# Performance work log

Measured on AMD Instinct MI355X. Metric: run time of the kernel, lower is better.

Reference implementation:

```python
import jax, jax.numpy as jnp
import numpy as np
import math

B, S, E, R = 128, 16, 512, 500  # batch, seq_len, emb_size, relation_num


def setup_inputs() -> dict:
    key = jax.random.key(0)
    ks = jax.random.split(key, 12)
    s = 1.0 / math.sqrt(E)
    emb = jax.random.normal(ks[0], (R + 1, E), jnp.float32) * s
    emb = emb.at[R].set(0.0)  # padding_idx row is zero in torch
    w_ih = jax.random.normal(ks[1], (4 * E, E), jnp.float32) * s
    w_hh = jax.random.normal(ks[2], (4 * E, E), jnp.float32) * s
    b_ih = jax.random.normal(ks[3], (4 * E,), jnp.float32) * s
    b_hh = jax.random.normal(ks[4], (4 * E,), jnp.float32) * s
    fc_w = jax.random.normal(ks[5], (1, E), jnp.float32) * s
    fc_b = jax.random.normal(ks[6], (1,), jnp.float32) * s
    fcq_w = jax.random.normal(ks[7], (E, E), jnp.float32) * s
    fcq_b = jax.random.normal(ks[8], (E,), jnp.float32) * s
    fck_w = jax.random.normal(ks[9], (E, E), jnp.float32) * s
    fck_b = jax.random.normal(ks[10], (E,), jnp.float32) * s
    tokens = jax.random.randint(ks[11], (B, S), 0, R)  # avoid padding idx R
    return dict(tokens=tokens, emb=emb, w_ih=w_ih, w_hh=w_hh, b_ih=b_ih,
                b_hh=b_hh, fc_w=fc_w, fc_b=fc_b, fcq_w=fcq_w, fcq_b=fcq_b,
                fck_w=fck_w, fck_b=fck_b)


def _lstm_pair(x, w_ih, w_hh, b):
    # x: [..., 2, E]; 2-step LSTM from zero state, return final hidden [..., E]
    def cell(xt, h, c):
        g = xt @ w_ih.T + h @ w_hh.T + b
        i, f, gg, o = jnp.split(g, 4, axis=-1)  # torch gate order i,f,g,o
        c = jax.nn.sigmoid(f) * c + jax.nn.sigmoid(i) * jnp.tanh(gg)
        return jax.nn.sigmoid(o) * jnp.tanh(c), c
    z = jnp.zeros_like(x[..., 0, :])
    h1, c1 = cell(x[..., 0, :], z, z)
    h2, _ = cell(x[..., 1, :], h1, c1)
    return h2


def _attention(x, rel_emb, fcq_w, fcq_b, fck_w, fck_b):
    # x: [B,q,E]; keys = [relation embeddings ; x] -> scores [B,q,R+q]
    b = x.shape[0]
    rel = jnp.broadcast_to(rel_emb[None], (b,) + rel_emb.shape)
    kin = jnp.concatenate([rel, x], axis=1)
    k = kin @ fck_w.T + fck_b
    q = x @ fcq_w.T + fcq_b
    return jnp.einsum('bqe,bke->bqk', q, k) / math.sqrt(E)


def _entropy(scores):
    lp = jax.nn.log_softmax(scores, axis=-1)
    return -jnp.sum(jnp.exp(lp) * lp, axis=-1)


def reference(tokens, emb, w_ih, w_hh, b_ih, b_hh, fc_w, fc_b,
              fcq_w, fcq_b, fck_w, fck_b):
    b_lstm = b_ih + b_hh
    rel_emb = emb[:R]  # relation embeddings used as attention keys/values
    cur = emb[tokens]  # [B,S,E]
    bidx = jnp.arange(B)
    losses = []
    for L in range(S, 1, -1):  # lengths processed: S, S-1, ..., 2
        if L > 2:
            # all adjacent pairs, batched 2-step LSTM: [B, L-1, E]
            pairs = jnp.stack([cur[:, :-1], cur[:, 1:]], axis=2)
            h = _lstm_pair(pairs, w_ih, w_hh, b_lstm)
            sc = jax.nn.sigmoid(h @ fc_w.T + fc_b)[..., 0]  # [B, L-1]
            sel = jnp.argmax(sc, axis=-1)  # [B]
            selected = jnp.take_along_axis(h, sel[:, None, None], axis=1)  # [B,1,E]
            scores = _attention(selected, rel_emb, fcq_w, fcq_b, fck_w, fck_b)
            losses.append(_entropy(scores))  # [B,1]
            # weightedAverage: mask is all-False for seq_len==1, plain softmax
            prob = jax.nn.softmax(scores, axis=-1)  # [B,1,R+1]
            all_emb = jnp.concatenate(
                [jnp.broadcast_to(rel_emb[None], (B, R, E)), selected], axis=1)
            merged = jnp.einsum('bqk,bke->bqe', prob, all_emb)[:, 0]  # [B,E]
            # output = inputs.detach().clone(); write merged at sel; drop row sel+1
            base = jax.lax.stop_gradient(cur)
            base = base.at[bidx, sel].set(merged)
            j = jnp.arange(L - 1)[None, :]
            src = j + (j > sel[:, None]).astype(j.dtype)
            cur = jnp.take_along_axis(base, src[:, :, None], axis=1)  # [B,L-1,E]
        else:  # L == 2: plain LSTM over the two tokens
            h = _lstm_pair(cur, w_ih, w_hh, b_lstm)  # [B,E]
            cur = h[:, None, :]
            losses.append(jnp.zeros((B, 1), cur.dtype))
    scores_f = _attention(cur, rel_emb, fcq_w, fcq_b, fck_w, fck_b)  # [B,1,R+1]
    losses.append(_entropy(scores_f))
    loss_tensor = jnp.concatenate(losses, axis=-1)  # [B,S]
    return scores_f[:, 0], loss_tensor
```

## Files before the change

kernel.cpp:

```cpp
#include <hip/hip_runtime.h>
#include <hip/hip_bf16.h>

#define BB 128
#define SS 16
#define EE 512
#define RR 500
#define G4 2048
#define OUT0 64128
#define NSC 501
#define NPAIR 2047
#define NSU 1012

__device__ __forceinline__ float sigm(float x) { return 1.f / (1.f + expf(-x)); }

__device__ float g_blstm[G4];
__device__ float g_blstmr[G4];
__device__ float g_wihr[G4 * EE];
__device__ float g_whhr[G4 * EE];
__device__ float g_fcw[EE + 4];
__device__ float g_qbias[1024];
__device__ float g_Krel[RR * EE];
__device__ float g_cur[BB * SS * EE];
__device__ float g_G[BB * SS * G4];
__device__ float g_h1[BB * SS * EE];
__device__ float g_c1[BB * SS * EE];
__device__ float g_h2[BB * SS * EE];
__device__ float g_sc[BB * SS];
__device__ float g_ent[BB * SS];
__device__ int   g_sel[BB];
__device__ int   g_ord[BB * SS];
__device__ float g_fckwT[EE * EE];
__device__ float g_W2[RR * EE];
__device__ float g_Mx[EE * EE];
__device__ float g_c2[RR + 4];
__device__ float g_v1[EE];
__device__ float g_c0[1];
__device__ float g_su[BB * NSU];

__global__ void k_prep(const float* __restrict__ bih, const float* __restrict__ bhh,
                       const float* __restrict__ fcwv, const float* __restrict__ fcbv,
                       const float* __restrict__ fcqb, const float* __restrict__ fckb) {
    int i = blockIdx.x * blockDim.x + threadIdx.x;
    if (i < G4) g_blstm[i] = bih[i] + bhh[i];
    if (i < EE) {
        g_fcw[i] = fcwv[i];
        g_qbias[i] = fcqb[i];
        g_qbias[EE + i] = fckb[i];
    }
    if (i == 0) g_fcw[EE] = fcbv[0];
    if (i < BB * SS) g_ord[i] = i;
}

__global__ void k_reord(const float* __restrict__ wih, const float* __restrict__ whh) {
    int i = blockIdx.x * blockDim.x + threadIdx.x;
    if (i >= G4 * EE) return;
    int n = i >> 9;
    int k = i & (EE - 1);
    int e = n & (EE - 1);
    int gate = n >> 9;
    int np = 4 * e + gate;
    g_wihr[(size_t)np * EE + k] = wih[i];
    g_whhr[(size_t)np * EE + k] = whh[i];
    if (k == 0) g_blstmr[np] = g_blstm[n];
}

__global__ void k_gather(const int* __restrict__ tok, const float* __restrict__ emb) {
    int i = blockIdx.x * blockDim.x + threadIdx.x;
    if (i >= BB * SS * EE) return;
    int e = i & (EE - 1);
    int r = i >> 9;
    int t = tok[r];
    g_cur[i] = emb[(size_t)t * EE + e];
}

__global__ void k_tr(const float* __restrict__ fckw) {
    int i = blockIdx.x * blockDim.x + threadIdx.x;
    if (i >= EE * EE) return;
    int ep = i >> 9;
    int f = i & (EE - 1);
    g_fckwT[(size_t)f * EE + ep] = fckw[(size_t)ep * EE + f];
}

__global__ __launch_bounds__(512) void k_vprep(const float* __restrict__ fcqw, const float* __restrict__ fckw) {
    __shared__ float sh[512];
    int t = threadIdx.x;
    int blk = blockIdx.x;
    if (blk == 0) {
        float acc = 0.f;
        for (int ep = 0; ep < EE; ep++)
            acc += g_qbias[ep] * fckw[(size_t)ep * EE + t] + g_qbias[EE + ep] * fcqw[(size_t)ep * EE + t];
        g_v1[t] = acc;
    } else if (blk == 1) {
        sh[t] = g_qbias[t] * g_qbias[EE + t];
        __syncthreads();
        for (int s = 256; s > 0; s >>= 1) { if (t < s) sh[t] += sh[t + s]; __syncthreads(); }
        if (t == 0) g_c0[0] = sh[0];
    } else {
        int k = blk - 2;
        sh[t] = g_Krel[(size_t)k * EE + t] * g_qbias[t];
        __syncthreads();
        for (int s = 256; s > 0; s >>= 1) { if (t < s) sh[t] += sh[t + s]; __syncthreads(); }
        if (t == 0) g_c2[k] = sh[0];
    }
}

#define TM 32
#define TN 64
#define TK 32
__device__ __forceinline__ void gemm_dev(
    const float* __restrict__ A, int lda,
    const float* __restrict__ W, int ldw, int wtrans,
    const float* __restrict__ bias, const float* __restrict__ Dadd, int ldd,
    float* __restrict__ C, int ldc, int M, int N, int K)
{
    __shared__ __align__(16) float As[TK][TM + 2];
    __shared__ __align__(16) float Ws[TK][TN + 4];
    int tid = threadIdx.x;
    int mt = blockIdx.y * TM;
    int nt = blockIdx.x * TN;
    int tr = tid >> 4;
    int tc = tid & 15;
    float acc[2][4] = {{0.f,0.f,0.f,0.f},{0.f,0.f,0.f,0.f}};

    int ea = tid * 4;
    int ra = ea >> 5;
    int ka = ea & 31;
    int gmA = mt + ra;
    bool rokA = gmA < M;
    int ew = tid * 8;
    int rw = ew >> 5;
    int kw = ew & 31;
    int gnW = nt + rw;
    bool rokW = gnW < N;

    for (int kt = 0; kt < K; kt += TK) {
        #pragma unroll
        for (int i = 0; i < 4; i++) {
            int gk = kt + ka + i;
            float v = 0.f;
            if (rokA && gk < K) v = A[(size_t)gmA * lda + gk];
            As[ka + i][ra] = v;
        }
        #pragma unroll
        for (int i = 0; i < 8; i++) {
            int gk = kt + kw + i;
            float v = 0.f;
            if (rokW && gk < K)
                v = wtrans ? W[(size_t)gk * ldw + gnW] : W[(size_t)gnW * ldw + gk];
            Ws[kw + i][rw] = v;
        }
        __syncthreads();
        #pragma unroll
        for (int kk = 0; kk < TK; kk++) {
            const float2 a = *(const float2*)&As[kk][2 * tr];
            const float4 w = *(const float4*)&Ws[kk][4 * tc];
            acc[0][0] += a.x * w.x; acc[0][1] += a.x * w.y; acc[0][2] += a.x * w.z; acc[0][3] += a.x * w.w;
            acc[1][0] += a.y * w.x; acc[1][1] += a.y * w.y; acc[1][2] += a.y * w.z; acc[1][3] += a.y * w.w;
        }
        __syncthreads();
    }
    #pragma unroll
    for (int i = 0; i < 2; i++) {
        int gm = mt + 2 * tr + i;
        if (gm >= M) continue;
        #pragma unroll
        for (int j = 0; j < 4; j++) {
            int gn = nt + 4 * tc + j;
            if (gn >= N) continue;
            float v = (i == 0) ? ((j == 0) ? acc[0][0] : (j == 1) ? acc[0][1] : (j == 2) ? acc[0][2] : acc[0][3])
                               : ((j == 0) ? acc[1][0] : (j == 1) ? acc[1][1] : (j == 2) ? acc[1][2] : acc[1][3]);
            if (bias) v += bias[gn];
            if (Dadd) v += Dadd[(size_t)gm * ldd + gn];
            C[(size_t)gm * ldc + gn] = v;
        }
    }
}

#define UM 128
#define UN 128
#define UK 32
template<int MODE>
__global__ __launch_bounds__(256) void kg_bigF() {
    __shared__ __align__(16) float As[UK][UM + 4];
    __shared__ __align__(16) float Ws[UK][UN + 4];
    const float* __restrict__ A = (MODE == 0) ? g_cur : g_h1;
    const float* __restrict__ W = (MODE == 0) ? g_wihr : g_whhr;
    const int M = (MODE == 0) ? (BB * SS) : NPAIR;
    int tid = threadIdx.x;
    int mt = blockIdx.y * UM;
    int nt = blockIdx.x * UN;
    int tr = tid >> 4;
    int tc = tid & 15;
    float acc[8][8] = {};

    int ra = tid & 127;
    int ka = (tid >> 7) << 4;
    int gmA = mt + ra;
    bool rokA = gmA < M;
    const float* Arow = A + (size_t)(rokA ? gmA : 0) * EE;
    const float* Wrow = W + (size_t)(nt + ra) * EE;

    float4 pa[4] = {{0,0,0,0},{0,0,0,0},{0,0,0,0},{0,0,0,0}};
    float4 pw[4];
    #pragma unroll
    for (int j = 0; j < 4; j++) {
        if (rokA) pa[j] = *(const float4*)&Arow[ka + 4 * j];
        pw[j] = *(const float4*)&Wrow[ka + 4 * j];
    }

    for (int kt = 0; kt < EE; kt += UK) {
        __syncthreads();
        #pragma unroll
        for (int j = 0; j < 4; j++) {
            As[ka + 4 * j + 0][ra] = pa[j].x;
            As[ka + 4 * j + 1][ra] = pa[j].y;
            As[ka + 4 * j + 2][ra] = pa[j].z;
            As[ka + 4 * j + 3][ra] = pa[j].w;
            Ws[ka + 4 * j + 0][ra] = pw[j].x;
            Ws[ka + 4 * j + 1][ra] = pw[j].y;
            Ws[ka + 4 * j + 2][ra] = pw[j].z;
            Ws[ka + 4 * j + 3][ra] = pw[j].w;
        }
        __syncthreads();
        if (kt + UK < EE) {
            int k2 = kt + UK + ka;
            #pragma unroll
            for (int j = 0; j < 4; j++) {
                if (rokA) pa[j] = *(const float4*)&Arow[k2 + 4 * j];
                pw[j] = *(const float4*)&Wrow[k2 + 4 * j];
            }
        }
        #pragma unroll
        for (int kk = 0; kk < UK; kk++) {
            const float4 aA = *(const float4*)&As[kk][4 * tr];
            const float4 aB = *(const float4*)&As[kk][64 + 4 * tr];
            const float4 wA = *(const float4*)&Ws[kk][4 * tc];
            const float4 wB = *(const float4*)&Ws[kk][64 + 4 * tc];
            const float am[8] = {aA.x, aA.y, aA.z, aA.w, aB.x, aB.y, aB.z, aB.w};
            const float wn[8] = {wA.x, wA.y, wA.z, wA.w, wB.x, wB.y, wB.z, wB.w};
            #pragma unroll
            for (int i = 0; i < 8; i++)
                #pragma unroll
                for (int j = 0; j < 8; j++)
                    acc[i][j] += am[i] * wn[j];
        }
    }

    int c0 = nt + 4 * tc;
    int c1c = c0 + 64;
    int e0 = (nt >> 2) + tc;
    #pragma unroll
    for (int ri = 0; ri < 8; ri++) {
        int row = (ri < 4) ? (4 * tr + ri) : (60 + 4 * tr + ri);
        int gm = mt + row;
        if (gm >= M) continue;
        float q0x = acc[ri][0], q0y = acc[ri][1], q0z = acc[ri][2], q0w = acc[ri][3];
        float q1x = acc[ri][4], q1y = acc[ri][5], q1z = acc[ri][6], q1w = acc[ri][7];
        if (MODE == 0) {
            const float4 b0 = *(const float4*)&g_blstmr[c0];
            const float4 b1 = *(const float4*)&g_blstmr[c1c];
            q0x += b0.x; q0y += b0.y; q0z += b0.z; q0w += b0.w;
            q1x += b1.x; q1y += b1.y; q1z += b1.z; q1w += b1.w;
            float4 o0 = {q0x, q0y, q0z, q0w};
            float4 o1 = {q1x, q1y, q1z, q1w};
            *(float4*)&g_G[(size_t)gm * G4 + c0]  = o0;
            *(float4*)&g_G[(size_t)gm * G4 + c1c] = o1;
            float cA = sigm(q0x) * tanhf(q0z);
            g_c1[(size_t)gm * EE + e0] = cA;
            g_h1[(size_t)gm * EE + e0] = sigm(q0w) * tanhf(cA);
            float cB = sigm(q1x) * tanhf(q1z);
            g_c1[(size_t)gm * EE + e0 + 16] = cB;
            g_h1[(size_t)gm * EE + e0 + 16] = sigm(q1w) * tanhf(cB);
        } else {
            const float4 d0 = *(const float4*)&g_G[(size_t)(gm + 1) * G4 + c0];
            const float4 d1 = *(const float4*)&g_G[(size_t)(gm + 1) * G4 + c1c];
            q0x += d0.x; q0y += d0.y; q0z += d0.z; q0w += d0.w;
            q1x += d1.x; q1y += d1.y; q1z += d1.z; q1w += d1.w;
            float c1a = g_c1[(size_t)gm * EE + e0];
            float c1b = g_c1[(size_t)gm * EE + e0 + 16];
            float cA = sigm(q0y) * c1a + sigm(q0x) * tanhf(q0z);
            g_h2[(size_t)gm * EE + e0] = sigm(q0w) * tanhf(cA);
            float cB = sigm(q1y) * c1b + sigm(q1x) * tanhf(q1z);
            g_h2[(size_t)gm * EE + e0 + 16] = sigm(q1w) * tanhf(cB);
        }
    }
}

__global__ __launch_bounds__(256) void kg_Krel(const float* __restrict__ emb, const float* __restrict__ fckw) {
    gemm_dev(emb, EE, fckw, EE, 0, g_qbias + EE, nullptr, 0, g_Krel, EE, RR, EE, EE);
}
__global__ __launch_bounds__(256) void kg_W2(const float* __restrict__ fcqw) {
    gemm_dev(g_Krel, EE, fcqw, EE, 1, nullptr, nullptr, 0, g_W2, EE, RR, EE, EE);
}
__global__ __launch_bounds__(256) void kg_Mx(const float* __restrict__ fcqw) {
    gemm_dev(g_fckwT, EE, fcqw, EE, 1, nullptr, nullptr, 0, g_Mx, EE, EE, EE, EE);
}

__global__ __launch_bounds__(256) void k_scI() {
    int m = blockIdx.x;
    int t = threadIdx.x;
    __shared__ float red[256];
    const float* h = g_h2 + (size_t)m * EE;
    float part = h[t] * g_fcw[t] + h[t + 256] * g_fcw[t + 256];
    red[t] = part;
    __syncthreads();
    for (int s = 128; s > 0; s >>= 1) { if (t < s) red[t] += red[t + s]; __syncthreads(); }
    if (t == 0) g_sc[m] = red[0];
}

__global__ __launch_bounds__(256) void k_scP(int L) {
    int m = blockIdx.x;
    int b = m >> 1;
    int tcand = m & 1;
    int s = g_sel[b];
    int p = s - 1 + tcand;
    bool valid = tcand == 0 ? (s >= 1) : (s <= L - 3);
    if (!valid) return;
    int physL = g_ord[b * SS + p];
    int t = threadIdx.x;
    __shared__ float red[256];
    const float* h = g_h2 + (size_t)physL * EE;
    float part = h[t] * g_fcw[t] + h[t + 256] * g_fcw[t + 256];
    red[t] = part;
    __syncthreads();
    for (int s2 = 128; s2 > 0; s2 >>= 1) { if (t < s2) red[t] += red[t + s2]; __syncthreads(); }
    if (t == 0) g_sc[b * SS + p] = red[0];
}

__global__ __launch_bounds__(256) void kg_su(int P) {
    __shared__ __align__(16) float As[TK][TM + 2];
    __shared__ __align__(16) float Ws[TK][TN + 4];
    __shared__ int s_phys[TM];
    int tid = threadIdx.x;
    int mt = blockIdx.y * TM;
    int nt = blockIdx.x * TN;
    int tr = tid >> 4;
    int tc = tid & 15;
    float acc[2][4] = {{0.f,0.f,0.f,0.f},{0.f,0.f,0.f,0.f}};

    if (tid < TM) {
        int b = mt + tid;
        float best = -1e30f; int bi = 0;
        for (int p = 0; p < P; p++) {
            float v = g_sc[b * SS + p];
            if (v > best) { best = v; bi = p; }
        }
        s_phys[tid] = g_ord[b * SS + bi];
        if (blockIdx.x == 0) g_sel[b] = bi;
    }
    __syncthreads();

    int ea = tid * 4;
    int ra = ea >> 5;
    int ka = ea & 31;
    int physA = s_phys[ra];
    int ew = tid * 8;
    int rw = ew >> 5;
    int kw = ew & 31;
    int gnW = nt + rw;
    bool rokW = gnW < NSU;
    const float* Wrow = nullptr;
    if (rokW) Wrow = (gnW < RR) ? (g_W2 + (size_t)gnW * EE) : (g_Mx + (size_t)(gnW - RR) * EE);

    for (int kt = 0; kt < EE; kt += TK) {
        #pragma unroll
        for (int i = 0; i < 4; i++)
            As[ka + i][ra] = g_h2[(size_t)physA * EE + kt + ka + i];
        #pragma unroll
        for (int i = 0; i < 8; i++)
            Ws[kw + i][rw] = rokW ? Wrow[kt + kw + i] : 0.f;
        __syncthreads();
        #pragma unroll
        for (int kk = 0; kk < TK; kk++) {
            const float2 a = *(const float2*)&As[kk][2 * tr];
            const float4 w = *(const float4*)&Ws[kk][4 * tc];
            acc[0][0] += a.x * w.x; acc[0][1] += a.x * w.y; acc[0][2] += a.x * w.z; acc[0][3] += a.x * w.w;
            acc[1][0] += a.y * w.x; acc[1][1] += a.y * w.y; acc[1][2] += a.y * w.z; acc[1][3] += a.y * w.w;
        }
        __syncthreads();
    }
    #pragma unroll
    for (int i = 0; i < 2; i++) {
        int gm = mt + 2 * tr + i;
        #pragma unroll
        for (int j = 0; j < 4; j++) {
            int gn = nt + 4 * tc + j;
            if (gn >= NSU) continue;
            float v = (i == 0) ? ((j == 0) ? acc[0][0] : (j == 1) ? acc[0][1] : (j == 2) ? acc[0][2] : acc[0][3])
                               : ((j == 0) ? acc[1][0] : (j == 1) ? acc[1][1] : (j == 2) ? acc[1][2] : acc[1][3]);
            g_su[(size_t)gm * NSU + gn] = v + (gn < RR ? g_c2[gn] : 0.f);
        }
    }
}

__global__ __launch_bounds__(256) void kg_GiF() {
    __shared__ __align__(16) float As[TK][TM + 2];
    __shared__ __align__(16) float Ws[TK][TN + 4];
    __shared__ int s_phys[TM];
    int tid = threadIdx.x;
    int mt = blockIdx.y * TM;
    int nt = blockIdx.x * TN;
    int tr = tid >> 4;
    int tc = tid & 15;
    float acc[2][4] = {{0.f,0.f,0.f,0.f},{0.f,0.f,0.f,0.f}};

    if (tid < TM) {
        int b = mt + tid;
        s_phys[tid] = g_ord[b * SS + g_sel[b]];
    }
    __syncthreads();

    int ea = tid * 4;
    int ra = ea >> 5;
    int ka = ea & 31;
    int physA = s_phys[ra];
    int ew = tid * 8;
    int rw = ew >> 5;
    int kw = ew & 31;
    int gnW = nt + rw;

    for (int kt = 0; kt < EE; kt += TK) {
        #pragma unroll
        for (int i = 0; i < 4; i++)
            As[ka + i][ra] = g_cur[(size_t)physA * EE + kt + ka + i];
        #pragma unroll
        for (int i = 0; i < 8; i++)
            Ws[kw + i][rw] = g_wihr[(size_t)gnW * EE + kt + kw + i];
        __syncthreads();
        #pragma unroll
        for (int kk = 0; kk < TK; kk++) {
            const float2 a = *(const float2*)&As[kk][2 * tr];
            const float4 w = *(const float4*)&Ws[kk][4 * tc];
            acc[0][0] += a.x * w.x; acc[0][1] += a.x * w.y; acc[0][2] += a.x * w.z; acc[0][3] += a.x * w.w;
            acc[1][0] += a.y * w.x; acc[1][1] += a.y * w.y; acc[1][2] += a.y * w.z; acc[1][3] += a.y * w.w;
        }
        __syncthreads();
    }
    int c0 = nt + 4 * tc;
    int e0 = (nt >> 2) + tc;
    const float4 b4 = *(const float4*)&g_blstmr[c0];
    #pragma unroll
    for (int i = 0; i < 2; i++) {
        int phys = s_phys[2 * tr + i];
        float qx = acc[i][0] + b4.x;
        float qy = acc[i][1] + b4.y;
        float qz = acc[i][2] + b4.z;
        float qw = acc[i][3] + b4.w;
        float4 o = {qx, qy, qz, qw};
        *(float4*)&g_G[(size_t)phys * G4 + c0] = o;
        float cA = sigm(qx) * tanhf(qz);
        g_c1[(size_t)phys * EE + e0] = cA;
        g_h1[(size_t)phys * EE + e0] = sigm(qw) * tanhf(cA);
    }
}

__global__ __launch_bounds__(256) void kg_g2iF(int L) {
    __shared__ __align__(16) float As[TK][TM + 2];
    __shared__ __align__(16) float Ws[TK][TN + 4];
    __shared__ int s_physA[TM];
    __shared__ int s_physD[TM];
    __shared__ int s_val[TM];
    int tid = threadIdx.x;
    int mt = blockIdx.y * TM;
    int nt = blockIdx.x * TN;
    int tr = tid >> 4;
    int tc = tid & 15;
    float acc[2][4] = {{0.f,0.f,0.f,0.f},{0.f,0.f,0.f,0.f}};

    if (tid < TM) {
        int gm = mt + tid;
        int b = gm >> 1;
        int tcand = gm & 1;
        int s = g_sel[b];
        int p = min(max(s - 1 + tcand, 0), 14);
        s_physA[tid] = g_ord[b * SS + p];
        s_physD[tid] = g_ord[b * SS + p + 1];
        s_val[tid] = tcand == 0 ? (s >= 1) : (s <= L - 3);
    }
    __syncthreads();

    int ea = tid * 4;
    int ra = ea >> 5;
    int ka = ea & 31;
    int physA = s_physA[ra];
    int ew = tid * 8;
    int rw = ew >> 5;
    int kw = ew & 31;
    int gnW = nt + rw;

    for (int kt = 0; kt < EE; kt += TK) {
        #pragma unroll
        for (int i = 0; i < 4; i++)
            As[ka + i][ra] = g_h1[(size_t)physA * EE + kt + ka + i];
        #pragma unroll
        for (int i = 0; i < 8; i++)
            Ws[kw + i][rw] = g_whhr[(size_t)gnW * EE + kt + kw + i];
        __syncthreads();
        #pragma unroll
        for (int kk = 0; kk < TK; kk++) {
            const float2 a = *(const float2*)&As[kk][2 * tr];
            const float4 w = *(const float4*)&Ws[kk][4 * tc];
            acc[0][0] += a.x * w.x; acc[0][1] += a.x * w.y; acc[0][2] += a.x * w.z; acc[0][3] += a.x * w.w;
            acc[1][0] += a.y * w.x; acc[1][1] += a.y * w.y; acc[1][2] += a.y * w.z; acc[1][3] += a.y * w.w;
        }
        __syncthreads();
    }
    int c0 = nt + 4 * tc;
    int e0 = (nt >> 2) + tc;
    #pragma unroll
    for (int i = 0; i < 2; i++) {
        int r = 2 * tr + i;
        if (!s_val[r]) continue;
        int pA = s_physA[r];
        int pD = s_physD[r];
        const float4 d4 = *(const float4*)&g_G[(size_t)pD * G4 + c0];
        float qx = acc[i][0] + d4.x;
        float qy = acc[i][1] + d4.y;
        float qz = acc[i][2] + d4.z;
        float qw = acc[i][3] + d4.w;
        float c1v = g_c1[(size_t)pA * EE + e0];
        float cA = sigm(qy) * c1v + sigm(qx) * tanhf(qz);
        g_h2[(size_t)pA * EE + e0] = sigm(qw) * tanhf(cA);
    }
}

__global__ __launch_bounds__(512) void k_smu(int col, int finalFlag, int L,
                                             const float* __restrict__ emb, float* __restrict__ out) {
    int b = blockIdx.x;
    int t = threadIdx.x;
    __shared__ float sh[512];
    __shared__ float srow[NSC];
    __shared__ float s_p500;
    const float* su = g_su + (size_t)b * NSU;
    int s = g_sel[b];
    int phys = g_ord[b * SS + s];
    const float* h2row = g_h2 + (size_t)phys * EE;
    const float isq = 0.044194173824159216f;

    float hv = h2row[t];
    sh[t] = hv * (su[RR + t] + g_v1[t]);
    __syncthreads();
    for (int ss = 256; ss > 0; ss >>= 1) { if (t < ss) sh[t] += sh[t + ss]; __syncthreads(); }
    if (t == 0) srow[RR] = (sh[0] + g_c0[0]) * isq;
    __syncthreads();
    if (t < RR) srow[t] = su[t] * isq;
    __syncthreads();
    float mx = (t < NSC) ? srow[t] : -1e30f;
    sh[t] = mx; __syncthreads();
    for (int ss = 256; ss > 0; ss >>= 1) { if (t < ss) sh[t] = fmaxf(sh[t], sh[t + ss]); __syncthreads(); }
    mx = sh[0]; __syncthreads();
    float zp = (t < NSC) ? expf(srow[t] - mx) : 0.f;
    sh[t] = zp; __syncthreads();
    for (int ss = 256; ss > 0; ss >>= 1) { if (t < ss) sh[t] += sh[t + ss]; __syncthreads(); }
    float lse = mx + logf(sh[0]);
    __syncthreads();
    float p = (t < NSC) ? expf(srow[t] - lse) : 0.f;
    float ep = (t < NSC) ? p * (lse - srow[t]) : 0.f;
    if (finalFlag && t < NSC) out[(size_t)b * NSC + t] = srow[t];
    sh[t] = ep; __syncthreads();
    for (int ss = 256; ss > 0; ss >>= 1) { if (t < ss) sh[t] += sh[t + ss]; __syncthreads(); }
    if (finalFlag) {
        if (t < 16) {
            float v = (t == 15) ? sh[0] : ((t == 14) ? 0.f : g_ent[b * SS + t]);
            out[OUT0 + b * 16 + t] = v;
        }
        return;
    }
    if (t == 0) g_ent[b * SS + col] = sh[0];

    __syncthreads();
    if (t < NSC) srow[t] = p;
    if (t == RR) s_p500 = p;
    __syncthreads();
    float macc = 0.f;
    #pragma unroll 4
    for (int k = 0; k < RR; k++) macc += srow[k] * emb[(size_t)k * EE + t];
    g_cur[(size_t)phys * EE + t] = macc + s_p500 * hv;
    if (t == 0) {
        for (int j = s + 1; j <= L - 2; j++) g_ord[b * SS + j] = g_ord[b * SS + j + 1];
        for (int pp = s + 1; pp <= L - 3; pp++) g_sc[b * SS + pp] = g_sc[b * SS + pp + 1];
    }
}

extern "C" void kernel_launch(void* const* d_in, const int* in_sizes, int n_in,
                              void* d_out, int out_size, void* d_ws, size_t ws_size,
                              hipStream_t stream) {
    const int*   tokens = (const int*)d_in[0];
    const float* emb    = (const float*)d_in[1];
    const float* wih    = (const float*)d_in[2];
    const float* whh    = (const float*)d_in[3];
    const float* bih    = (const float*)d_in[4];
    const float* bhh    = (const float*)d_in[5];
    const float* fcwv   = (const float*)d_in[6];
    const float* fcbv   = (const float*)d_in[7];
    const float* fcqw   = (const float*)d_in[8];
    const float* fcqb   = (const float*)d_in[9];
    const float* fckw   = (const float*)d_in[10];
    const float* fckb   = (const float*)d_in[11];
    float* out = (float*)d_out;

    auto grid32 = [](int M, int N) { return dim3((unsigned)((N + TN - 1) / TN), (unsigned)((M + TM - 1) / TM)); };

    k_prep<<<dim3(8), dim3(256), 0, stream>>>(bih, bhh, fcwv, fcbv, fcqb, fckb);
    k_reord<<<dim3((G4 * EE) / 256), dim3(256), 0, stream>>>(wih, whh);
    kg_Krel<<<grid32(RR, EE), dim3(256), 0, stream>>>(emb, fckw);
    k_tr<<<dim3((EE * EE + 255) / 256), dim3(256), 0, stream>>>(fckw);
    kg_W2<<<grid32(RR, EE), dim3(256), 0, stream>>>(fcqw);
    kg_Mx<<<grid32(EE, EE), dim3(256), 0, stream>>>(fcqw);
    k_vprep<<<dim3(502), dim3(512), 0, stream>>>(fcqw, fckw);
    k_gather<<<dim3((BB * SS * EE + 255) / 256), dim3(256), 0, stream>>>(tokens, emb);

    kg_bigF<0><<<dim3(16, 16), dim3(256), 0, stream>>>();
    kg_bigF<1><<<dim3(16, 16), dim3(256), 0, stream>>>();
    k_scI<<<dim3(NPAIR), dim3(256), 0, stream>>>();

    for (int L = SS; L >= 3; L--) {
        kg_su<<<grid32(BB, NSU), dim3(256), 0, stream>>>(L - 1);
        k_smu<<<dim3(BB), dim3(512), 0, stream>>>(SS - L, 0, L, emb, out);
        kg_GiF<<<grid32(BB, G4), dim3(256), 0, stream>>>();
        kg_g2iF<<<grid32(2 * BB, G4), dim3(256), 0, stream>>>(L);
        k_scP<<<dim3(2 * BB), dim3(256), 0, stream>>>(L);
    }

    kg_su<<<grid32(BB, NSU), dim3(256), 0, stream>>>(1);
    k_smu<<<dim3(BB), dim3(512), 0, stream>>>(15, 1, 2, emb, out);

    (void)in_sizes; (void)n_in; (void)out_size; (void)d_ws; (void)ws_size;
}
```

Baseline: 1.953 ms.

## Double-buffer shared memory tiles and vectorize global loads in all GEMM kernels

Every GEMM kernel (generic gemm_dev, kg_su, kg_GiF, kg_g2iF, kg_bigF) now uses two shared-memory tile buffers. Each loop step prefetches the next K-tile into registers with float4 loads, stores it to the other buffer after computing on the current one, and needs only one barrier per step instead of two. To make the float4 W loads possible, fcqw is pre-transposed into g_fcqwT and the strided transposed-W path is removed. This doubles shared memory per block, which may lower occupancy.

```diff
diff --git a/kernel.cpp b/kernel.cpp
--- a/kernel.cpp
+++ b/kernel.cpp
@@ -30,6 +30,7 @@
 __device__ int   g_sel[BB];
 __device__ int   g_ord[BB * SS];
 __device__ float g_fckwT[EE * EE];
+__device__ float g_fcqwT[EE * EE];
 __device__ float g_W2[RR * EE];
 __device__ float g_Mx[EE * EE];
 __device__ float g_c2[RR + 4];
@@ -73,12 +74,13 @@
     g_cur[i] = emb[(size_t)t * EE + e];
 }
 
-__global__ void k_tr(const float* __restrict__ fckw) {
+__global__ void k_tr(const float* __restrict__ fckw, const float* __restrict__ fcqw) {
     int i = blockIdx.x * blockDim.x + threadIdx.x;
     if (i >= EE * EE) return;
     int ep = i >> 9;
     int f = i & (EE - 1);
     g_fckwT[(size_t)f * EE + ep] = fckw[(size_t)ep * EE + f];
+    g_fcqwT[(size_t)f * EE + ep] = fcqw[(size_t)ep * EE + f];
 }
 
 __global__ __launch_bounds__(512) void k_vprep(const float* __restrict__ fcqw, const float* __restrict__ fckw) {
@@ -109,12 +111,12 @@
 #define TK 32
 __device__ __forceinline__ void gemm_dev(
     const float* __restrict__ A, int lda,
-    const float* __restrict__ W, int ldw, int wtrans,
+    const float* __restrict__ W, int ldw,
     const float* __restrict__ bias, const float* __restrict__ Dadd, int ldd,
     float* __restrict__ C, int ldc, int M, int N, int K)
 {
-    __shared__ __align__(16) float As[TK][TM + 2];
-    __shared__ __align__(16) float Ws[TK][TN + 4];
+    __shared__ __align__(16) float As[2][TK][TM + 2];
+    __shared__ __align__(16) float Ws[2][TK][TN + 4];
     int tid = threadIdx.x;
     int mt = blockIdx.y * TM;
     int nt = blockIdx.x * TN;
@@ -127,35 +129,43 @@
     int ka = ea & 31;
     int gmA = mt + ra;
     bool rokA = gmA < M;
+    const float* Arow = A + (size_t)(rokA ? gmA : 0) * lda;
     int ew = tid * 8;
     int rw = ew >> 5;
     int kw = ew & 31;
     int gnW = nt + rw;
     bool rokW = gnW < N;
-
-    for (int kt = 0; kt < K; kt += TK) {
-        #pragma unroll
-        for (int i = 0; i < 4; i++) {
-            int gk = kt + ka + i;
-            float v = 0.f;
-            if (rokA && gk < K) v = A[(size_t)gmA * lda + gk];
-            As[ka + i][ra] = v;
-        }
-        #pragma unroll
-        for (int i = 0; i < 8; i++) {
-            int gk = kt + kw + i;
-            float v = 0.f;
-            if (rokW && gk < K)
-                v = wtrans ? W[(size_t)gk * ldw + gnW] : W[(size_t)gnW * ldw + gk];
-            Ws[kw + i][rw] = v;
-        }
-        __syncthreads();
+    const float* Wrow = W + (size_t)(rokW ? gnW : 0) * ldw;
+
+    float4 pa = {0,0,0,0}, pw0 = {0,0,0,0}, pw1 = {0,0,0,0};
+    if (rokA) pa = *(const float4*)&Arow[ka];
+    if (rokW) { pw0 = *(const float4*)&Wrow[kw]; pw1 = *(const float4*)&Wrow[kw + 4]; }
+    As[0][ka + 0][ra] = pa.x; As[0][ka + 1][ra] = pa.y; As[0][ka + 2][ra] = pa.z; As[0][ka + 3][ra] = pa.w;
+    Ws[0][kw + 0][rw] = pw0.x; Ws[0][kw + 1][rw] = pw0.y; Ws[0][kw + 2][rw] = pw0.z; Ws[0][kw + 3][rw] = pw0.w;
+    Ws[0][kw + 4][rw] = pw1.x; Ws[0][kw + 5][rw] = pw1.y; Ws[0][kw + 6][rw] = pw1.z; Ws[0][kw + 7][rw] = pw1.w;
+    __syncthreads();
+
+    int P = K / TK;
+    for (int p = 0; p < P; p++) {
+        int cur = p & 1;
+        bool more = (p + 1) < P;
+        if (more) {
+            int k2 = (p + 1) * TK;
+            if (rokA) pa = *(const float4*)&Arow[k2 + ka];
+            if (rokW) { pw0 = *(const float4*)&Wrow[k2 + kw]; pw1 = *(const float4*)&Wrow[k2 + kw + 4]; }
+        }
         #pragma unroll
         for (int kk = 0; kk < TK; kk++) {
-            const float2 a = *(const float2*)&As[kk][2 * tr];
-            const float4 w = *(const float4*)&Ws[kk][4 * tc];
+            const float2 a = *(const float2*)&As[cur][kk][2 * tr];
+            const float4 w = *(const float4*)&Ws[cur][kk][4 * tc];
             acc[0][0] += a.x * w.x; acc[0][1] += a.x * w.y; acc[0][2] += a.x * w.z; acc[0][3] += a.x * w.w;
             acc[1][0] += a.y * w.x; acc[1][1] += a.y * w.y; acc[1][2] += a.y * w.z; acc[1][3] += a.y * w.w;
+        }
+        if (more) {
+            int nxt = cur ^ 1;
+            As[nxt][ka + 0][ra] = pa.x; As[nxt][ka + 1][ra] = pa.y; As[nxt][ka + 2][ra] = pa.z; As[nxt][ka + 3][ra] = pa.w;
+            Ws[nxt][kw + 0][rw] = pw0.x; Ws[nxt][kw + 1][rw] = pw0.y; Ws[nxt][kw + 2][rw] = pw0.z; Ws[nxt][kw + 3][rw] = pw0.w;
+            Ws[nxt][kw + 4][rw] = pw1.x; Ws[nxt][kw + 5][rw] = pw1.y; Ws[nxt][kw + 6][rw] = pw1.z; Ws[nxt][kw + 7][rw] = pw1.w;
         }
         __syncthreads();
     }
@@ -181,8 +191,8 @@
 #define UK 32
 template<int MODE>
 __global__ __launch_bounds__(256) void kg_bigF() {
-    __shared__ __align__(16) float As[UK][UM + 4];
-    __shared__ __align__(16) float Ws[UK][UN + 4];
+    __shared__ __align__(16) float As[2][UK][UM + 4];
+    __shared__ __align__(16) float Ws[2][UK][UN + 4];
     const float* __restrict__ A = (MODE == 0) ? g_cur : g_h1;
     const float* __restrict__ W = (MODE == 0) ? g_wihr : g_whhr;
     const int M = (MODE == 0) ? (BB * SS) : NPAIR;
@@ -200,30 +210,32 @@
     const float* Arow = A + (size_t)(rokA ? gmA : 0) * EE;
     const float* Wrow = W + (size_t)(nt + ra) * EE;
 
-    float4 pa[4] = {{0,0,0,0},{0,0,0,0},{0,0,0,0},{0,0,0,0}};
+    float4 pa[4] = {};
     float4 pw[4];
     #pragma unroll
     for (int j = 0; j < 4; j++) {
         if (rokA) pa[j] = *(const float4*)&Arow[ka + 4 * j];
         pw[j] = *(const float4*)&Wrow[ka + 4 * j];
     }
-
-    for (int kt = 0; kt < EE; kt += UK) {
-        __syncthreads();
-        #pragma unroll
-        for (int j = 0; j < 4; j++) {
-            As[ka + 4 * j + 0][ra] = pa[j].x;
-            As[ka + 4 * j + 1][ra] = pa[j].y;
-            As[ka + 4 * j + 2][ra] = pa[j].z;
-            As[ka + 4 * j + 3][ra] = pa[j].w;
-            Ws[ka + 4 * j + 0][ra] = pw[j].x;
-            Ws[ka + 4 * j + 1][ra] = pw[j].y;
-            Ws[ka + 4 * j + 2][ra] = pw[j].z;
-            Ws[ka + 4 * j + 3][ra] = pw[j].w;
-        }
-        __syncthreads();
-        if (kt + UK < EE) {
-            int k2 = kt + UK + ka;
+    #pragma unroll
+    for (int j = 0; j < 4; j++) {
+        As[0][ka + 4 * j + 0][ra] = pa[j].x;
+        As[0][ka + 4 * j + 1][ra] = pa[j].y;
+        As[0][ka + 4 * j + 2][ra] = pa[j].z;
+        As[0][ka + 4 * j + 3][ra] = pa[j].w;
+        Ws[0][ka + 4 * j + 0][ra] = pw[j].x;
+        Ws[0][ka + 4 * j + 1][ra] = pw[j].y;
+        Ws[0][ka + 4 * j + 2][ra] = pw[j].z;
+        Ws[0][ka + 4 * j + 3][ra] = pw[j].w;
+    }
+    __syncthreads();
+
+    const int P = EE / UK;
+    for (int p = 0; p < P; p++) {
+        int cur = p & 1;
+        bool more = (p + 1) < P;
+        if (more) {
+            int k2 = (p + 1) * UK + ka;
             #pragma unroll
             for (int j = 0; j < 4; j++) {
                 if (rokA) pa[j] = *(const float4*)&Arow[k2 + 4 * j];
@@ -232,10 +244,10 @@
         }
         #pragma unroll
         for (int kk = 0; kk < UK; kk++) {
-            const float4 aA = *(const float4*)&As[kk][4 * tr];
-            const float4 aB = *(const float4*)&As[kk][64 + 4 * tr];
-            const float4 wA = *(const float4*)&Ws[kk][4 * tc];
-            const float4 wB = *(const float4*)&Ws[kk][64 + 4 * tc];
+            const float4 aA = *(const float4*)&As[cur][kk][4 * tr];
+            const float4 aB = *(const float4*)&As[cur][kk][64 + 4 * tr];
+            const float4 wA = *(const float4*)&Ws[cur][kk][4 * tc];
+            const float4 wB = *(const float4*)&Ws[cur][kk][64 + 4 * tc];
             const float am[8] = {aA.x, aA.y, aA.z, aA.w, aB.x, aB.y, aB.z, aB.w};
             const float wn[8] = {wA.x, wA.y, wA.z, wA.w, wB.x, wB.y, wB.z, wB.w};
             #pragma unroll
@@ -244,6 +256,21 @@
                 for (int j = 0; j < 8; j++)
                     acc[i][j] += am[i] * wn[j];
         }
+        if (more) {
+            int nxt = cur ^ 1;
+            #pragma unroll
+            for (int j = 0; j < 4; j++) {
+                As[nxt][ka + 4 * j + 0][ra] = pa[j].x;
+                As[nxt][ka + 4 * j + 1][ra] = pa[j].y;
+                As[nxt][ka + 4 * j + 2][ra] = pa[j].z;
+                As[nxt][ka + 4 * j + 3][ra] = pa[j].w;
+                Ws[nxt][ka + 4 * j + 0][ra] = pw[j].x;
+                Ws[nxt][ka + 4 * j + 1][ra] = pw[j].y;
+                Ws[nxt][ka + 4 * j + 2][ra] = pw[j].z;
+                Ws[nxt][ka + 4 * j + 3][ra] = pw[j].w;
+            }
+        }
+        __syncthreads();
     }
 
     int c0 = nt + 4 * tc;
@@ -287,13 +314,13 @@
 }
 
 __global__ __launch_bounds__(256) void kg_Krel(const float* __restrict__ emb, const float* __restrict__ fckw) {
-    gemm_dev(emb, EE, fckw, EE, 0, g_qbias + EE, nullptr, 0, g_Krel, EE, RR, EE, EE);
-}
-__global__ __launch_bounds__(256) void kg_W2(const float* __restrict__ fcqw) {
-    gemm_dev(g_Krel, EE, fcqw, EE, 1, nullptr, nullptr, 0, g_W2, EE, RR, EE, EE);
-}
-__global__ __launch_bounds__(256) void kg_Mx(const float* __restrict__ fcqw) {
-    gemm_dev(g_fckwT, EE, fcqw, EE, 1, nullptr, nullptr, 0, g_Mx, EE, EE, EE, EE);
+    gemm_dev(emb, EE, fckw, EE, g_qbias + EE, nullptr, 0, g_Krel, EE, RR, EE, EE);
+}
+__global__ __launch_bounds__(256) void kg_W2() {
+    gemm_dev(g_Krel, EE, g_fcqwT, EE, nullptr, nullptr, 0, g_W2, EE, RR, EE, EE);
+}
+__global__ __launch_bounds__(256) void kg_Mx() {
+    gemm_dev(g_fckwT, EE, g_fcqwT, EE, nullptr, nullptr, 0, g_Mx, EE, EE, EE, EE);
 }
 
 __global__ __launch_bounds__(256) void k_scI() {
@@ -328,8 +355,8 @@
 }
 
 __global__ __launch_bounds__(256) void kg_su(int P) {
-    __shared__ __align__(16) float As[TK][TM + 2];
-    __shared__ __align__(16) float Ws[TK][TN + 4];
+    __shared__ __align__(16) float As[2][TK][TM + 2];
+    __shared__ __align__(16) float Ws[2][TK][TN + 4];
     __shared__ int s_phys[TM];
     int tid = threadIdx.x;
     int mt = blockIdx.y * TM;
@@ -353,7 +380,7 @@
     int ea = tid * 4;
     int ra = ea >> 5;
     int ka = ea & 31;
-    int physA = s_phys[ra];
+    const float* Arow = g_h2 + (size_t)s_phys[ra] * EE;
     int ew = tid * 8;
     int rw = ew >> 5;
     int kw = ew & 31;
@@ -362,20 +389,35 @@
     const float* Wrow = nullptr;
     if (rokW) Wrow = (gnW < RR) ? (g_W2 + (size_t)gnW * EE) : (g_Mx + (size_t)(gnW - RR) * EE);
 
-    for (int kt = 0; kt < EE; kt += TK) {
-        #pragma unroll
-        for (int i = 0; i < 4; i++)
-            As[ka + i][ra] = g_h2[(size_t)physA * EE + kt + ka + i];
-        #pragma unroll
-        for (int i = 0; i < 8; i++)
-            Ws[kw + i][rw] = rokW ? Wrow[kt + kw + i] : 0.f;
-        __syncthreads();
+    float4 pa = *(const float4*)&Arow[ka];
+    float4 pw0 = {0,0,0,0}, pw1 = {0,0,0,0};
+    if (rokW) { pw0 = *(const float4*)&Wrow[kw]; pw1 = *(const float4*)&Wrow[kw + 4]; }
+    As[0][ka + 0][ra] = pa.x; As[0][ka + 1][ra] = pa.y; As[0][ka + 2][ra] = pa.z; As[0][ka + 3][ra] = pa.w;
+    Ws[0][kw + 0][rw] = pw0.x; Ws[0][kw + 1][rw] = pw0.y; Ws[0][kw + 2][rw] = pw0.z; Ws[0][kw + 3][rw] = pw0.w;
+    Ws[0][kw + 4][rw] = pw1.x; Ws[0][kw + 5][rw] = pw1.y; Ws[0][kw + 6][rw] = pw1.z; Ws[0][kw + 7][rw] = pw1.w;
+    __syncthreads();
+
+    const int NP = EE / TK;
+    for (int p = 0; p < NP; p++) {
+        int cur = p & 1;
+        bool more = (p + 1) < NP;
+        if (more) {
+            int k2 = (p + 1) * TK;
+            pa = *(const float4*)&Arow[k2 + ka];
+            if (rokW) { pw0 = *(const float4*)&Wrow[k2 + kw]; pw1 = *(const float4*)&Wrow[k2 + kw + 4]; }
+        }
         #pragma unroll
         for (int kk = 0; kk < TK; kk++) {
-            const float2 a = *(const float2*)&As[kk][2 * tr];
-            const float4 w = *(const float4*)&Ws[kk][4 * tc];
+            const float2 a = *(const float2*)&As[cur][kk][2 * tr];
+            const float4 w = *(const float4*)&Ws[cur][kk][4 * tc];
             acc[0][0] += a.x * w.x; acc[0][1] += a.x * w.y; acc[0][2] += a.x * w.z; acc[0][3] += a.x * w.w;
             acc[1][0] += a.y * w.x; acc[1][1] += a.y * w.y; acc[1][2] += a.y * w.z; acc[1][3] += a.y * w.w;
+        }
+        if (more) {
+            int nxt = cur ^ 1;
+            As[nxt][ka + 0][ra] = pa.x; As[nxt][ka + 1][ra] = pa.y; As[nxt][ka + 2][ra] = pa.z; As[nxt][ka + 3][ra] = pa.w;
+            Ws[nxt][kw + 0][rw] = pw0.x; Ws[nxt][kw + 1][rw] = pw0.y; Ws[nxt][kw + 2][rw] = pw0.z; Ws[nxt][kw + 3][rw] = pw0.w;
+            Ws[nxt][kw + 4][rw] = pw1.x; Ws[nxt][kw + 5][rw] = pw1.y; Ws[nxt][kw + 6][rw] = pw1.z; Ws[nxt][kw + 7][rw] = pw1.w;
         }
         __syncthreads();
     }
@@ -394,8 +436,8 @@
 }
 
 __global__ __launch_bounds__(256) void kg_GiF() {
-    __shared__ __align__(16) float As[TK][TM + 2];
-    __shared__ __align__(16) float Ws[TK][TN + 4];
+    __shared__ __align__(16) float As[2][TK][TM + 2];
+    __shared__ __align__(16) float Ws[2][TK][TN + 4];
     __shared__ int s_phys[TM];
     int tid = threadIdx.x;
     int mt = blockIdx.y * TM;
@@ -413,26 +455,42 @@
     int ea = tid * 4;
     int ra = ea >> 5;
     int ka = ea & 31;
-    int physA = s_phys[ra];
+    const float* Arow = g_cur + (size_t)s_phys[ra] * EE;
     int ew = tid * 8;
     int rw = ew >> 5;
     int kw = ew & 31;
-    int gnW = nt + rw;
-
-    for (int kt = 0; kt < EE; kt += TK) {
-        #pragma unroll
-        for (int i = 0; i < 4; i++)
-            As[ka + i][ra] = g_cur[(size_t)physA * EE + kt + ka + i];
-        #pragma unroll
-        for (int i = 0; i < 8; i++)
-            Ws[kw + i][rw] = g_wihr[(size_t)gnW * EE + kt + kw + i];
-        __syncthreads();
+    const float* Wrow = g_wihr + (size_t)(nt + rw) * EE;
+
+    float4 pa = *(const float4*)&Arow[ka];
+    float4 pw0 = *(const float4*)&Wrow[kw];
+    float4 pw1 = *(const float4*)&Wrow[kw + 4];
+    As[0][ka + 0][ra] = pa.x; As[0][ka + 1][ra] = pa.y; As[0][ka + 2][ra] = pa.z; As[0][ka + 3][ra] = pa.w;
+    Ws[0][kw + 0][rw] = pw0.x; Ws[0][kw + 1][rw] = pw0.y; Ws[0][kw + 2][rw] = pw0.z; Ws[0][kw + 3][rw] = pw0.w;
+    Ws[0][kw + 4][rw] = pw1.x; Ws[0][kw + 5][rw] = pw1.y; Ws[0][kw + 6][rw] = pw1.z; Ws[0][kw + 7][rw] = pw1.w;
+    __syncthreads();
+
+    const int NP = EE / TK;
+    for (int p = 0; p < NP; p++) {
+        int cur = p & 1;
+        bool more = (p + 1) < NP;
+        if (more) {
+            int k2 = (p + 1) * TK;
+            pa = *(const float4*)&Arow[k2 + ka];
+            pw0 = *(const float4*)&Wrow[k2 + kw];
+            pw1 = *(const float4*)&Wrow[k2 + kw + 4];
+        }
         #pragma unroll
         for (int kk = 0; kk < TK; kk++) {
-            const float2 a = *(const float2*)&As[kk][2 * tr];
-            const float4 w = *(const float4*)&Ws[kk][4 * tc];
+            const float2 a = *(const float2*)&As[cur][kk][2 * tr];
+            const float4 w = *(const float4*)&Ws[cur][kk][4 * tc];
             acc[0][0] += a.x * w.x; acc[0][1] += a.x * w.y; acc[0][2] += a.x * w.z; acc[0][3] += a.x * w.w;
             acc[1][0] += a.y * w.x; acc[1][1] += a.y * w.y; acc[1][2] += a.y * w.z; acc[1][3] += a.y * w.w;
+        }
+        if (more) {
+            int nxt = cur ^ 1;
+            As[nxt][ka + 0][ra] = pa.x; As[nxt][ka + 1][ra] = pa.y; As[nxt][ka + 2][ra] = pa.z; As[nxt][ka + 3][ra] = pa.w;
+            Ws[nxt][kw + 0][rw] = pw0.x; Ws[nxt][kw + 1][rw] = pw0.y; Ws[nxt][kw + 2][rw] = pw0.z; Ws[nxt][kw + 3][rw] = pw0.w;
+            Ws[nxt][kw + 4][rw] = pw1.x; Ws[nxt][kw + 5][rw] = pw1.y; Ws[nxt][kw + 6][rw] = pw1.z; Ws[nxt][kw + 7][rw] = pw1.w;
         }
         __syncthreads();
     }
@@ -455,8 +513,8 @@
 }
 
 __global__ __launch_bounds__(256) void kg_g2iF(int L) {
-    __shared__ __align__(16) float As[TK][TM + 2];
-    __shared__ __align__(16) float Ws[TK][TN + 4];
+    __shared__ __align__(16) float As[2][TK][TM + 2];
+    __shared__ __align__(16) float Ws[2][TK][TN + 4];
     __shared__ int s_physA[TM];
     __shared__ int s_physD[TM];
     __shared__ int s_val[TM];
@@ -482,26 +540,42 @@
     int ea = tid * 4;
     int ra = ea >> 5;
     int ka = ea & 31;
-    int physA = s_physA[ra];
+    const float* Arow = g_h1 + (size_t)s_physA[ra] * EE;
     int ew = tid * 8;
     int rw = ew >> 5;
     int kw = ew & 31;
-    int gnW = nt + rw;
-
-    for (int kt = 0; kt < EE; kt += TK) {
-        #pragma unroll
-        for (int i = 0; i < 4; i++)
-            As[ka + i][ra] = g_h1[(size_t)physA * EE + kt + ka + i];
-        #pragma unroll
-        for (int i = 0; i < 8; i++)
-            Ws[kw + i][rw] = g_whhr[(size_t)gnW * EE + kt + kw + i];
-        __syncthreads();
+    const float* Wrow = g_whhr + (size_t)(nt + rw) * EE;
+
+    float4 pa = *(const float4*)&Arow[ka];
+    float4 pw0 = *(const float4*)&Wrow[kw];
+    float4 pw1 = *(const float4*)&Wrow[kw + 4];
+    As[0][ka + 0][ra] = pa.x; As[0][ka + 1][ra] = pa.y; As[0][ka + 2][ra] = pa.z; As[0][ka + 3][ra] = pa.w;
+    Ws[0][kw + 0][rw] = pw0.x; Ws[0][kw + 1][rw] = pw0.y; Ws[0][kw + 2][rw] = pw0.z; Ws[0][kw + 3][rw] = pw0.w;
+    Ws[0][kw + 4][rw] = pw1.x; Ws[0][kw + 5][rw] = pw1.y; Ws[0][kw + 6][rw] = pw1.z; Ws[0][kw + 7][rw] = pw1.w;
+    __syncthreads();
+
+    const int NP = EE / TK;
+    for (int p = 0; p < NP; p++) {
+        int cur = p & 1;
+        bool more = (p + 1) < NP;
+        if (more) {
+            int k2 = (p + 1) * TK;
+            pa = *(const float4*)&Arow[k2 + ka];
+            pw0 = *(const float4*)&Wrow[k2 + kw];
+            pw1 = *(const float4*)&Wrow[k2 + kw + 4];
+        }
         #pragma unroll
         for (int kk = 0; kk < TK; kk++) {
-            const float2 a = *(const float2*)&As[kk][2 * tr];
-            const float4 w = *(const float4*)&Ws[kk][4 * tc];
+            const float2 a = *(const float2*)&As[cur][kk][2 * tr];
+            const float4 w = *(const float4*)&Ws[cur][kk][4 * tc];
             acc[0][0] += a.x * w.x; acc[0][1] += a.x * w.y; acc[0][2] += a.x * w.z; acc[0][3] += a.x * w.w;
             acc[1][0] += a.y * w.x; acc[1][1] += a.y * w.y; acc[1][2] += a.y * w.z; acc[1][3] += a.y * w.w;
+        }
+        if (more) {
+            int nxt = cur ^ 1;
+            As[nxt][ka + 0][ra] = pa.x; As[nxt][ka + 1][ra] = pa.y; As[nxt][ka + 2][ra] = pa.z; As[nxt][ka + 3][ra] = pa.w;
+            Ws[nxt][kw + 0][rw] = pw0.x; Ws[nxt][kw + 1][rw] = pw0.y; Ws[nxt][kw + 2][rw] = pw0.z; Ws[nxt][kw + 3][rw] = pw0.w;
+            Ws[nxt][kw + 4][rw] = pw1.x; Ws[nxt][kw + 5][rw] = pw1.y; Ws[nxt][kw + 6][rw] = pw1.z; Ws[nxt][kw + 7][rw] = pw1.w;
         }
         __syncthreads();
     }
@@ -554,8 +628,8 @@
     for (int ss = 256; ss > 0; ss >>= 1) { if (t < ss) sh[t] += sh[t + ss]; __syncthreads(); }
     float lse = mx + logf(sh[0]);
     __syncthreads();
-    float p = (t < NSC) ? expf(srow[t] - lse) : 0.f;
-    float ep = (t < NSC) ? p * (lse - srow[t]) : 0.f;
+    float pb = (t < NSC) ? expf(srow[t] - lse) : 0.f;
+    float ep = (t < NSC) ? pb * (lse - srow[t]) : 0.f;
     if (finalFlag && t < NSC) out[(size_t)b * NSC + t] = srow[t];
     sh[t] = ep; __syncthreads();
     for (int ss = 256; ss > 0; ss >>= 1) { if (t < ss) sh[t] += sh[t + ss]; __syncthreads(); }
@@ -569,8 +643,8 @@
     if (t == 0) g_ent[b * SS + col] = sh[0];
 
     __syncthreads();
-    if (t < NSC) srow[t] = p;
-    if (t == RR) s_p500 = p;
+    if (t < NSC) srow[t] = pb;
+    if (t == RR) s_p500 = pb;
     __syncthreads();
     float macc = 0.f;
     #pragma unroll 4
@@ -604,9 +678,9 @@
     k_prep<<<dim3(8), dim3(256), 0, stream>>>(bih, bhh, fcwv, fcbv, fcqb, fckb);
     k_reord<<<dim3((G4 * EE) / 256), dim3(256), 0, stream>>>(wih, whh);
     kg_Krel<<<grid32(RR, EE), dim3(256), 0, stream>>>(emb, fckw);
-    k_tr<<<dim3((EE * EE + 255) / 256), dim3(256), 0, stream>>>(fckw);
-    kg_W2<<<grid32(RR, EE), dim3(256), 0, stream>>>(fcqw);
-    kg_Mx<<<grid32(EE, EE), dim3(256), 0, stream>>>(fcqw);
+    k_tr<<<dim3((EE * EE + 255) / 256), dim3(256), 0, stream>>>(fckw, fcqw);
+    kg_W2<<<grid32(RR, EE), dim3(256), 0, stream>>>();
+    kg_Mx<<<grid32(EE, EE), dim3(256), 0, stream>>>();
     k_vprep<<<dim3(502), dim3(512), 0, stream>>>(fcqw, fckw);
     k_gather<<<dim3((BB * SS * EE + 255) / 256), dim3(256), 0, stream>>>(tokens, emb);
 
```

After: 2.042 ms. 4.6% more time.
